# Performance work log

Measured on AMD Instinct MI355X. Metric: run time of the kernel, lower is better.

The kernel has to match this reference:

```python
import jax, jax.numpy as jnp
import numpy as np
from jax import lax

B, N, C, RED = 8, 2048, 1024, 4
GN_EPS = 1e-5


def setup_inputs() -> dict:
    key = jax.random.key(0)
    ks = jax.random.split(key, 8)
    s = lambda k, shp, sc: jax.random.normal(k, shp, jnp.float32) * sc
    return dict(
        x=jax.random.normal(ks[0], (B, N, C), jnp.float32),
        qkv_w=s(ks[1], (C, 3 * C), 0.02),
        c1=jnp.float32(0.01 ** 2),
        c2=jnp.float32(0.03 ** 2),
        conv1_w=s(ks[2], (4, 1, 3), 0.3),      # OIH
        gn_g=jnp.ones(4, jnp.float32),
        gn_b=jnp.zeros(4, jnp.float32),
        conv2_w=s(ks[3], (1, 4, 3), 0.3),      # OIH
        conv2_b=jnp.zeros(1, jnp.float32),
        ch_w1=s(ks[4], (C, C // RED), 0.02),
        ch_b1=jnp.zeros(C // RED, jnp.float32),
        ch_w2=s(ks[5], (C // RED, C), 0.02),
        ch_b2=jnp.zeros(C, jnp.float32),
        proj_w=s(ks[6], (C, C), 0.02),
        proj_b=jnp.zeros(C, jnp.float32),
    )


def _conv1d(x, w):  # x:[B,Cin,N], w:[O,I,3], pad=1
    return lax.conv_general_dilated(x, w, (1,), [(1, 1)],
                                    dimension_numbers=('NCH', 'OIH', 'NCH'))


def _ode_func(A, conv1_w, gn_g, gn_b, conv2_w, conv2_b):
    # A: [B,N] -> Conv1d(1,4) -> GroupNorm(2,4) -> ReLU -> Conv1d(4,1)
    h = _conv1d(A[:, None, :], conv1_w)                 # [B,4,N]
    b, _, n = h.shape
    hg = h.reshape(b, 2, 2, n)                          # 2 groups of 2 channels
    mu = hg.mean((2, 3), keepdims=True)
    var = hg.var((2, 3), keepdims=True)
    h = ((hg - mu) * lax.rsqrt(var + GN_EPS)).reshape(b, 4, n)
    h = jax.nn.relu(h * gn_g[None, :, None] + gn_b[None, :, None])
    y = _conv1d(h, conv2_w) + conv2_b[None, :, None]    # [B,1,N]
    return y[:, 0, :]


def reference(x, qkv_w, c1, c2, conv1_w, gn_g, gn_b, conv2_w, conv2_b,
              ch_w1, ch_b1, ch_w2, ch_b2, proj_w, proj_b):
    Bx, Nx, Cx = x.shape
    qkv = (x @ qkv_w).reshape(Bx, Nx, 3, Cx)
    q, k, v = qkv[..., 0, :], qkv[..., 1, :], qkv[..., 2, :]

    # SSIM-style per-token statistics over the channel dim
    mu_q = q.mean(-1, keepdims=True)
    mu_k = k.mean(-1, keepdims=True)
    dq, dk = q - mu_q, k - mu_k
    inv_cm1 = 1.0 / (Cx - 1)
    sigma_qk = (dq * dk).sum(-1, keepdims=True) * inv_cm1
    sigma_q2 = (dq * dq).sum(-1, keepdims=True) * inv_cm1
    sigma_k2 = (dk * dk).sum(-1, keepdims=True) * inv_cm1
    num = (2 * mu_q * mu_k + c1) * (2 * sigma_qk + c2)
    den = (mu_q ** 2 + mu_k ** 2 + c1) * (sigma_q2 + sigma_k2 + c2)
    attn_base = ((num / (den + 1e-7)) ** 2)[..., 0]     # [B,N]

    # explicit-Euler integration over t = linspace(0,1,2) -> one step, dt=1
    steps = 2
    ts = jnp.linspace(0.0, 1.0, steps)
    dts = ts[1:] - ts[:-1]

    def step(A, dt):
        return A + dt * _ode_func(A, conv1_w, gn_g, gn_b, conv2_w, conv2_b), None

    A, _ = lax.scan(step, attn_base, dts)
    final_a = jax.nn.sigmoid(A)                         # [B,N]
    weights = jax.nn.softmax(final_a, axis=1)           # softmax over tokens

    # channel gating from mean token
    m = x.mean(axis=1, keepdims=True)                   # [B,1,C]
    ch_w = jax.nn.sigmoid(jax.nn.relu(m @ ch_w1 + ch_b1) @ ch_w2 + ch_b2)

    out_low = weights[..., None] * v * ch_w             # [B,N,C]
    return out_low @ proj_w + proj_b
```

## Files before the change

kernel.cpp:

```cpp
#include <hip/hip_runtime.h>

typedef __attribute__((ext_vector_type(8))) short short8;
typedef __attribute__((ext_vector_type(4))) short short4v;
typedef __attribute__((ext_vector_type(4))) float floatx4;

__device__ __forceinline__ unsigned short f2bf(float f) {
    unsigned u = __float_as_uint(f);
    u = u + 0x7fffu + ((u >> 16) & 1u);
    return (unsigned short)(u >> 16);
}
__device__ __forceinline__ float bf2f(short s) {
    return __uint_as_float(((unsigned)(unsigned short)s) << 16);
}

__device__ __forceinline__ void gl_lds16(const void* g, void* l) {
    __builtin_amdgcn_global_load_lds((const __attribute__((address_space(1))) void*)g,
                                     (__attribute__((address_space(3))) void*)l, 16, 0, 0);
}

__global__ __launch_bounds__(256) void convmean_kernel(const float* __restrict__ x,
                                                       short* __restrict__ xb,
                                                       float* __restrict__ part) {
    int bid = blockIdx.x;
    int b = bid >> 6, nch = bid & 63;
    int tid = threadIdx.x;
    size_t base = ((size_t)b * 2048 + nch * 32) * 1024;
    float s0 = 0.f, s1 = 0.f, s2 = 0.f, s3 = 0.f;
    int c0 = tid * 4;
    for (int r = 0; r < 32; r++) {
        const float* rp = x + base + (size_t)r * 1024 + c0;
        float4 v = *(const float4*)rp;
        s0 += v.x; s1 += v.y; s2 += v.z; s3 += v.w;
        short4v o;
        o[0] = (short)f2bf(v.x); o[1] = (short)f2bf(v.y);
        o[2] = (short)f2bf(v.z); o[3] = (short)f2bf(v.w);
        *(short4v*)(xb + base + (size_t)r * 1024 + c0) = o;
    }
    float* pp = part + ((size_t)b * 64 + nch) * 1024 + c0;
    float4 ps; ps.x = s0; ps.y = s1; ps.z = s2; ps.w = s3;
    *(float4*)pp = ps;
}

__global__ __launch_bounds__(256) void transpose_conv_kernel(const float* __restrict__ w_qkv,
                                                             short* __restrict__ qkvT,
                                                             const float* __restrict__ w_proj,
                                                             short* __restrict__ projT) {
    __shared__ float t[64][65];
    int bx = blockIdx.x;
    const float* in; short* out; int C; bool is_qkv;
    int c0, r0 = blockIdx.y * 64;
    if (bx < 48) { in = w_qkv; out = qkvT; C = 3072; c0 = bx * 64; is_qkv = true; }
    else         { in = w_proj; out = projT; C = 1024; c0 = (bx - 48) * 64; is_qkv = false; }
    int tid = threadIdx.x;
#pragma unroll
    for (int l = 0; l < 16; l++) {
        int idx = l * 256 + tid;
        int rr = idx >> 6, cc = idx & 63;
        t[rr][cc] = in[(size_t)(r0 + rr) * C + c0 + cc];
    }
    __syncthreads();
#pragma unroll
    for (int l = 0; l < 16; l++) {
        int idx = l * 256 + tid;
        int rr = idx >> 6, cc = idx & 63;
        int ro = c0 + rr;
        int rnew = ro;
        if (is_qkv) {
            if (ro < 1024) rnew = 2 * ro;
            else if (ro < 2048) rnew = 2 * (ro - 1024) + 1;
        }
        out[(size_t)rnew * 1024 + r0 + cc] = (short)f2bf(t[cc][rr]);
    }
}

__global__ __launch_bounds__(256) void ch_kernel(const float* __restrict__ part,
                                                 const float* __restrict__ w1,
                                                 const float* __restrict__ b1,
                                                 const float* __restrict__ w2,
                                                 const float* __restrict__ b2,
                                                 float* __restrict__ ch) {
    int b = blockIdx.x >> 3, cg = blockIdx.x & 7;
    int tid = threadIdx.x;
    __shared__ float mrow[1024];
    __shared__ float hid[256];
    for (int i = tid; i < 1024; i += 256) {
        float s = 0.f;
        for (int j = 0; j < 64; j++) s += part[((size_t)b * 64 + j) * 1024 + i];
        mrow[i] = s * (1.f / 2048.f);
    }
    __syncthreads();
    {
        float s0 = 0.f, s1 = 0.f, s2 = 0.f, s3 = 0.f;
        for (int i = 0; i < 1024; i += 4) {
            s0 += mrow[i] * w1[(size_t)i * 256 + tid];
            s1 += mrow[i + 1] * w1[(size_t)(i + 1) * 256 + tid];
            s2 += mrow[i + 2] * w1[(size_t)(i + 2) * 256 + tid];
            s3 += mrow[i + 3] * w1[(size_t)(i + 3) * 256 + tid];
        }
        hid[tid] = fmaxf((s0 + s1) + (s2 + s3) + b1[tid], 0.f);
    }
    __syncthreads();
    if (tid < 128) {
        int c = cg * 128 + tid;
        float s0 = 0.f, s1 = 0.f, s2 = 0.f, s3 = 0.f;
        for (int j = 0; j < 256; j += 4) {
            s0 += hid[j] * w2[(size_t)j * 1024 + c];
            s1 += hid[j + 1] * w2[(size_t)(j + 1) * 1024 + c];
            s2 += hid[j + 2] * w2[(size_t)(j + 2) * 1024 + c];
            s3 += hid[j + 3] * w2[(size_t)(j + 3) * 1024 + c];
        }
        float s = (s0 + s1) + (s2 + s3) + b2[c];
        ch[(size_t)b * 1024 + c] = 1.f / (1.f + expf(-s));
    }
}

__global__ __launch_bounds__(256, 4) void gemm_qkv_kernel(const short* __restrict__ A,
                                                          const short* __restrict__ BT,
                                                          short* __restrict__ vbuf,
                                                          const float* __restrict__ ch,
                                                          float* __restrict__ part2)
{
    __shared__ __align__(16) short Ash[2 * 128 * 32];
    __shared__ __align__(16) short Bsh[2 * 128 * 32];
    const int tid = threadIdx.x;
    const int wave = tid >> 6, lane = tid & 63;
    const int id = blockIdx.x;
    const int xcd = id & 7, j = id >> 3;
    const int half = j / 192;
    const int rem = j % 192;
    const int bmi = rem & 7;
    const int bn = rem >> 3;
    const int bm = (half * 8 + bmi) * 8 + xcd;
    const int wm = wave >> 1, wn = wave & 1;
    const int l4 = lane >> 2, kk = (lane & 3) * 8;
    const int lda = 1024, ldb = 1024;

    const short* Ag = A + (size_t)(bm * 128 + wave * 32 + l4) * lda + kk;
    const short* Bg = BT + (size_t)(bn * 128 + wave * 32 + l4) * ldb + kk;
    short* lA = Ash + wave * 1024;
    short* lB = Bsh + wave * 1024;

    floatx4 acc[4][4];
    floatx4 zero = {0.f, 0.f, 0.f, 0.f};
#pragma unroll
    for (int i = 0; i < 4; i++)
#pragma unroll
        for (int jj = 0; jj < 4; jj++) acc[i][jj] = zero;

    const int ar = lane & 15, ak = (lane >> 4) * 8;
    const int quad = lane >> 4;

    for (int k0 = 0; k0 < 1024; k0 += 64) {
#pragma unroll
        for (int h = 0; h < 2; h++) {
            gl_lds16(Ag + k0 + h * 32, lA + h * 4096);
            gl_lds16(Ag + 16 * lda + k0 + h * 32, lA + h * 4096 + 512);
            gl_lds16(Bg + k0 + h * 32, lB + h * 4096);
            gl_lds16(Bg + 16 * ldb + k0 + h * 32, lB + h * 4096 + 512);
        }
        __syncthreads();
#pragma unroll
        for (int h = 0; h < 2; h++) {
            short8 af[4], bfr[4];
#pragma unroll
            for (int t = 0; t < 4; t++)
                af[t] = *(const short8*)(Ash + h * 4096 + (wm * 64 + t * 16 + ar) * 32 + ak);
#pragma unroll
            for (int t = 0; t < 4; t++)
                bfr[t] = *(const short8*)(Bsh + h * 4096 + (wn * 64 + t * 16 + ar) * 32 + ak);
#pragma unroll
            for (int i = 0; i < 4; i++)
#pragma unroll
                for (int jj = 0; jj < 4; jj++)
                    acc[i][jj] = __builtin_amdgcn_mfma_f32_16x16x32_bf16(af[i], bfr[jj], acc[i][jj], 0, 0, 0);
        }
        __syncthreads();
    }

    if (bn < 16) {
        float* sb = (float*)Ash;
#pragma unroll
        for (int i = 0; i < 4; i++) {
            float st[4][5];
#pragma unroll
            for (int r = 0; r < 4; r++)
#pragma unroll
                for (int f = 0; f < 5; f++) st[r][f] = 0.f;
#pragma unroll
            for (int jj = 0; jj < 4; jj++) {
#pragma unroll
                for (int r = 0; r < 4; r++) {
                    float val = acc[i][jj][r];
                    float other = __shfl_xor(val, 1);
                    float q = (lane & 1) ? other : val;
                    float kv = (lane & 1) ? val : other;
                    st[r][0] += q; st[r][1] += kv;
                    st[r][2] += q * q; st[r][3] += kv * kv; st[r][4] += q * kv;
                }
            }
#pragma unroll
            for (int r = 0; r < 4; r++)
#pragma unroll
                for (int f = 0; f < 5; f++) {
                    float v = st[r][f];
                    v += __shfl_xor(v, 2);
                    v += __shfl_xor(v, 4);
                    v += __shfl_xor(v, 8);
                    st[r][f] = v;
                }
            if ((lane & 15) == 0) {
#pragma unroll
                for (int r = 0; r < 4; r++)
#pragma unroll
                    for (int f = 0; f < 5; f++)
                        sb[(size_t)(wn * 128 + wm * 64 + i * 16 + quad * 4 + r) * 5 + f] = st[r][f];
            }
        }
        __syncthreads();
        if (tid < 128) {
            int grow = bm * 128 + tid;
#pragma unroll
            for (int f = 0; f < 5; f++) {
                float s = sb[(size_t)tid * 5 + f] + sb[(size_t)(128 + tid) * 5 + f];
                part2[(size_t)(bn * 5 + f) * 16384 + grow] = s;
            }
        }
    } else {
        const int batch = (bm * 128) >> 11;
        const int vcol0 = bn * 128 - 2048 + wn * 64;
        short* pbuf = Ash + wave * 1024;
        float cw[4];
#pragma unroll
        for (int jj = 0; jj < 4; jj++) cw[jj] = ch[(size_t)batch * 1024 + vcol0 + jj * 16 + ar];
#pragma unroll
        for (int i = 0; i < 4; i++) {
#pragma unroll
            for (int jj = 0; jj < 4; jj++)
#pragma unroll
                for (int r = 0; r < 4; r++)
                    pbuf[(quad * 4 + r) * 64 + jj * 16 + ar] = (short)f2bf(acc[i][jj][r] * cw[jj]);
#pragma unroll
            for (int p = 0; p < 2; p++) {
                int idx = p * 512 + lane * 8;
                short8 vv = *(const short8*)(pbuf + idx);
                int grow = bm * 128 + wm * 64 + i * 16 + (idx >> 6);
                int gcol = vcol0 + (idx & 63);
                *(short8*)(vbuf + (size_t)grow * 1024 + gcol) = vv;
            }
        }
    }
}

__global__ __launch_bounds__(256) void finalize_kernel(const float* __restrict__ part2,
                                                       const float* __restrict__ c1p,
                                                       const float* __restrict__ c2p,
                                                       float* __restrict__ attn) {
    int row = blockIdx.x * 256 + threadIdx.x;
    float s[5] = {0.f, 0.f, 0.f, 0.f, 0.f};
#pragma unroll
    for (int slot = 0; slot < 16; slot++)
#pragma unroll
        for (int f = 0; f < 5; f++)
            s[f] += part2[(size_t)((slot * 5 + f) << 14) + row];
    const float C = 1024.f, invcm1 = 1.f / 1023.f;
    float c1 = *c1p, c2 = *c2p;
    float muq = s[0] / C, muk = s[1] / C;
    float sigqk = (s[4] - C * muq * muk) * invcm1;
    float sigq2 = (s[2] - C * muq * muq) * invcm1;
    float sigk2 = (s[3] - C * muk * muk) * invcm1;
    float num = (2.f * muq * muk + c1) * (2.f * sigqk + c2);
    float den = (muq * muq + muk * muk + c1) * (sigq2 + sigk2 + c2);
    float r = num / (den + 1e-7f);
    attn[row] = r * r;
}

__device__ __forceinline__ float blk_sum(float v, float* buf) {
#pragma unroll
    for (int m = 1; m < 64; m <<= 1) v += __shfl_xor(v, m);
    int wave = threadIdx.x >> 6;
    if ((threadIdx.x & 63) == 0) buf[wave] = v;
    __syncthreads();
    float r = buf[0] + buf[1] + buf[2] + buf[3];
    __syncthreads();
    return r;
}
__device__ __forceinline__ float blk_max(float v, float* buf) {
#pragma unroll
    for (int m = 1; m < 64; m <<= 1) v = fmaxf(v, __shfl_xor(v, m));
    int wave = threadIdx.x >> 6;
    if ((threadIdx.x & 63) == 0) buf[wave] = v;
    __syncthreads();
    float r = fmaxf(fmaxf(buf[0], buf[1]), fmaxf(buf[2], buf[3]));
    __syncthreads();
    return r;
}

__global__ __launch_bounds__(256) void ode_softmax_kernel(const float* __restrict__ attn,
                                                          const float* __restrict__ w1,
                                                          const float* __restrict__ gng,
                                                          const float* __restrict__ gnb,
                                                          const float* __restrict__ w2,
                                                          const float* __restrict__ b2,
                                                          float* __restrict__ wgt) {
    int b = blockIdx.x, tid = threadIdx.x;
    __shared__ float A0[2048];
    __shared__ float H[4][2048];
    __shared__ float rbuf[4];
    for (int i = tid; i < 2048; i += 256) A0[i] = attn[(size_t)b * 2048 + i];
    __syncthreads();
    float w1l[12], w2l[12];
#pragma unroll
    for (int i = 0; i < 12; i++) { w1l[i] = w1[i]; w2l[i] = w2[i]; }
    float gg[4], gb[4];
#pragma unroll
    for (int c = 0; c < 4; c++) { gg[c] = gng[c]; gb[c] = gnb[c]; }

    float s0 = 0.f, ss0 = 0.f, s1 = 0.f, ss1 = 0.f;
    for (int i = tid; i < 2048; i += 256) {
        float le = (i > 0) ? A0[i - 1] : 0.f;
        float mi = A0[i];
        float ri = (i < 2047) ? A0[i + 1] : 0.f;
#pragma unroll
        for (int c = 0; c < 4; c++) {
            float h = w1l[c * 3] * le + w1l[c * 3 + 1] * mi + w1l[c * 3 + 2] * ri;
            H[c][i] = h;
            if (c < 2) { s0 += h; ss0 += h * h; } else { s1 += h; ss1 += h * h; }
        }
    }
    s0 = blk_sum(s0, rbuf);
    ss0 = blk_sum(ss0, rbuf);
    s1 = blk_sum(s1, rbuf);
    ss1 = blk_sum(ss1, rbuf);
    float mu0 = s0 / 4096.f, var0 = ss0 / 4096.f - mu0 * mu0;
    float mu1 = s1 / 4096.f, var1 = ss1 / 4096.f - mu1 * mu1;
    float is0 = 1.f / sqrtf(var0 + 1e-5f);
    float is1 = 1.f / sqrtf(var1 + 1e-5f);

    for (int i = tid; i < 2048; i += 256) {
#pragma unroll
        for (int c = 0; c < 4; c++) {
            float inv = (c < 2) ? is0 : is1;
            float mu = (c < 2) ? mu0 : mu1;
            float v = (H[c][i] - mu) * inv * gg[c] + gb[c];
            H[c][i] = fmaxf(v, 0.f);
        }
    }
    __syncthreads();

    float bias2 = b2[0];
    float myfa[8];
    float lmax = -1e30f;
#pragma unroll
    for (int ii = 0; ii < 8; ii++) {
        int i = tid + ii * 256;
        float y = bias2;
#pragma unroll
        for (int c = 0; c < 4; c++) {
            float le = (i > 0) ? H[c][i - 1] : 0.f;
            float mi = H[c][i];
            float ri = (i < 2047) ? H[c][i + 1] : 0.f;
            y += w2l[c * 3] * le + w2l[c * 3 + 1] * mi + w2l[c * 3 + 2] * ri;
        }
        float Av = A0[i] + y;
        float fa = 1.f / (1.f + expf(-Av));
        myfa[ii] = fa;
        lmax = fmaxf(lmax, fa);
    }
    float gmax = blk_max(lmax, rbuf);
    float lsum = 0.f;
#pragma unroll
    for (int ii = 0; ii < 8; ii++) {
        myfa[ii] = expf(myfa[ii] - gmax);
        lsum += myfa[ii];
    }
    float gsum = blk_sum(lsum, rbuf);
    float inv = 1.f / gsum;
#pragma unroll
    for (int ii = 0; ii < 8; ii++) wgt[(size_t)b * 2048 + tid + ii * 256] = myfa[ii] * inv;
}

__global__ __launch_bounds__(256, 4) void gemm_out_kernel(const short* __restrict__ vbuf,
                                                          const short* __restrict__ BT,
                                                          const float* __restrict__ wgt,
                                                          const float* __restrict__ pb,
                                                          float* __restrict__ Out)
{
    __shared__ __align__(16) short Ash[2 * 128 * 32];
    __shared__ __align__(16) short Bsh[2 * 128 * 32];
    const int tid = threadIdx.x;
    const int wave = tid >> 6, lane = tid & 63;
    const int id = blockIdx.x;
    const int xcd = id & 7, j = id >> 3;
    const int half = j >> 6;
    const int rem = j & 63;
    const int bmi = rem & 7;
    const int bn = rem >> 3;
    const int bm = (half * 8 + bmi) * 8 + xcd;
    const int wm = wave >> 1, wn = wave & 1;
    const int l4 = lane >> 2, kk = (lane & 3) * 8;
    const int lda = 1024, ldb = 1024;

    const short* Ag = vbuf + (size_t)(bm * 128 + wave * 32 + l4) * lda + kk;
    const short* Bg = BT + (size_t)(bn * 128 + wave * 32 + l4) * ldb + kk;
    short* lA = Ash + wave * 1024;
    short* lB = Bsh + wave * 1024;

    floatx4 acc[4][4];
    floatx4 zero = {0.f, 0.f, 0.f, 0.f};
#pragma unroll
    for (int i = 0; i < 4; i++)
#pragma unroll
        for (int jj = 0; jj < 4; jj++) acc[i][jj] = zero;

    const int ar = lane & 15, ak = (lane >> 4) * 8;
    const int quad = lane >> 4;

    for (int k0 = 0; k0 < 1024; k0 += 64) {
#pragma unroll
        for (int h = 0; h < 2; h++) {
            gl_lds16(Ag + k0 + h * 32, lA + h * 4096);
            gl_lds16(Ag + 16 * lda + k0 + h * 32, lA + h * 4096 + 512);
            gl_lds16(Bg + k0 + h * 32, lB + h * 4096);
            gl_lds16(Bg + 16 * ldb + k0 + h * 32, lB + h * 4096 + 512);
        }
        __syncthreads();
#pragma unroll
        for (int h = 0; h < 2; h++) {
            short8 af[4], bfr[4];
#pragma unroll
            for (int t = 0; t < 4; t++)
                af[t] = *(const short8*)(Ash + h * 4096 + (wm * 64 + t * 16 + ar) * 32 + ak);
#pragma unroll
            for (int t = 0; t < 4; t++)
                bfr[t] = *(const short8*)(Bsh + h * 4096 + (wn * 64 + t * 16 + ar) * 32 + ak);
#pragma unroll
            for (int i = 0; i < 4; i++)
#pragma unroll
                for (int jj = 0; jj < 4; jj++)
                    acc[i][jj] = __builtin_amdgcn_mfma_f32_16x16x32_bf16(af[i], bfr[jj], acc[i][jj], 0, 0, 0);
        }
        __syncthreads();
    }

    const int row0 = bm * 128 + wm * 64;
    const int col0 = bn * 128 + wn * 64;
    float* obuf = (float*)Ash + wave * 1024;
#pragma unroll
    for (int i = 0; i < 4; i++) {
#pragma unroll
        for (int jj = 0; jj < 4; jj++) {
            float bias = pb[col0 + jj * 16 + ar];
#pragma unroll
            for (int r = 0; r < 4; r++) {
                int grow = row0 + i * 16 + quad * 4 + r;
                obuf[(quad * 4 + r) * 64 + jj * 16 + ar] = wgt[grow] * acc[i][jj][r] + bias;
            }
        }
#pragma unroll
        for (int p = 0; p < 4; p++) {
            int idx = p * 256 + lane * 4;
            float4 vv = *(const float4*)(obuf + idx);
            int grow = row0 + i * 16 + (idx >> 6);
            int gcol = col0 + (idx & 63);
            *(float4*)(Out + (size_t)grow * 1024 + gcol) = vv;
        }
    }
}

extern "C" void kernel_launch(void* const* d_in, const int* in_sizes, int n_in,
                              void* d_out, int out_size, void* d_ws, size_t ws_size,
                              hipStream_t stream) {
    const float* x       = (const float*)d_in[0];
    const float* qkv_w   = (const float*)d_in[1];
    const float* c1      = (const float*)d_in[2];
    const float* c2      = (const float*)d_in[3];
    const float* conv1_w = (const float*)d_in[4];
    const float* gn_g    = (const float*)d_in[5];
    const float* gn_b    = (const float*)d_in[6];
    const float* conv2_w = (const float*)d_in[7];
    const float* conv2_b = (const float*)d_in[8];
    const float* ch_w1   = (const float*)d_in[9];
    const float* ch_b1   = (const float*)d_in[10];
    const float* ch_w2   = (const float*)d_in[11];
    const float* ch_b2   = (const float*)d_in[12];
    const float* proj_w  = (const float*)d_in[13];
    const float* proj_b  = (const float*)d_in[14];
    float* out = (float*)d_out;

    size_t off = 0;
    char* base = (char*)d_ws;
    auto carve = [&](size_t bytes) -> char* {
        char* p = base + off;
        off += (bytes + 255) & ~(size_t)255;
        return p;
    };
    short* x_bf  = (short*)carve((size_t)16384 * 1024 * 2);
    short* qkvT  = (short*)carve((size_t)3072 * 1024 * 2);
    short* projT = (short*)carve((size_t)1024 * 1024 * 2);
    short* vbuf  = (short*)carve((size_t)16384 * 1024 * 2);
    float* part2 = (float*)carve((size_t)80 * 16384 * 4);
    float* attn  = (float*)carve((size_t)16384 * 4);
    float* wgt   = (float*)carve((size_t)16384 * 4);
    float* part  = (float*)carve((size_t)8 * 64 * 1024 * 4);
    float* chw   = (float*)carve((size_t)8 * 1024 * 4);

    convmean_kernel<<<512, 256, 0, stream>>>(x, x_bf, part);
    transpose_conv_kernel<<<dim3(64, 16), 256, 0, stream>>>(qkv_w, qkvT, proj_w, projT);
    ch_kernel<<<64, 256, 0, stream>>>(part, ch_w1, ch_b1, ch_w2, ch_b2, chw);
    gemm_qkv_kernel<<<3072, 256, 0, stream>>>(x_bf, qkvT, vbuf, chw, part2);
    finalize_kernel<<<64, 256, 0, stream>>>(part2, c1, c2, attn);
    ode_softmax_kernel<<<8, 256, 0, stream>>>(attn, conv1_w, gn_g, gn_b, conv2_w, conv2_b, wgt);
    gemm_out_kernel<<<1024, 256, 0, stream>>>(vbuf, projT, wgt, proj_b, out);
}
```

Measured before the change: 387.3 us.

## Fold V projection and channel gate into per-batch output weight matrix

Rather than computing V = x@Wv for all tokens and then projecting, the code precomputes a per-batch matrix M_b = Wv·diag(ch_b)·Wproj (8 small 1024^3 GEMMs) and multiplies x directly by it in the output GEMM. The QKV GEMM shrinks to Q and K only, and the bf16 V buffer write and read are gone. The cost is extra small GEMMs plus an added bf16 rounding of the fused matrix, which changes numerical error characteristics.

```diff
diff --git a/kernel.cpp b/kernel.cpp
--- a/kernel.cpp
+++ b/kernel.cpp
@@ -8,9 +8,6 @@
     unsigned u = __float_as_uint(f);
     u = u + 0x7fffu + ((u >> 16) & 1u);
     return (unsigned short)(u >> 16);
-}
-__device__ __forceinline__ float bf2f(short s) {
-    return __uint_as_float(((unsigned)(unsigned short)s) << 16);
 }
 
 __device__ __forceinline__ void gl_lds16(const void* g, void* l) {
@@ -49,8 +46,8 @@
     int bx = blockIdx.x;
     const float* in; short* out; int C; bool is_qkv;
     int c0, r0 = blockIdx.y * 64;
-    if (bx < 48) { in = w_qkv; out = qkvT; C = 3072; c0 = bx * 64; is_qkv = true; }
-    else         { in = w_proj; out = projT; C = 1024; c0 = (bx - 48) * 64; is_qkv = false; }
+    if (bx < 32) { in = w_qkv; out = qkvT; C = 3072; c0 = bx * 64; is_qkv = true; }
+    else         { in = w_proj; out = projT; C = 1024; c0 = (bx - 32) * 64; is_qkv = false; }
     int tid = threadIdx.x;
 #pragma unroll
     for (int l = 0; l < 16; l++) {
@@ -65,10 +62,7 @@
         int rr = idx >> 6, cc = idx & 63;
         int ro = c0 + rr;
         int rnew = ro;
-        if (is_qkv) {
-            if (ro < 1024) rnew = 2 * ro;
-            else if (ro < 2048) rnew = 2 * (ro - 1024) + 1;
-        }
+        if (is_qkv) rnew = (ro < 1024) ? 2 * ro : 2 * (ro - 1024) + 1;
         out[(size_t)rnew * 1024 + r0 + cc] = (short)f2bf(t[cc][rr]);
     }
 }
@@ -114,11 +108,106 @@
     }
 }
 
-__global__ __launch_bounds__(256, 4) void gemm_qkv_kernel(const short* __restrict__ A,
-                                                          const short* __restrict__ BT,
-                                                          short* __restrict__ vbuf,
-                                                          const float* __restrict__ ch,
-                                                          float* __restrict__ part2)
+__global__ __launch_bounds__(256) void scale_wv_kernel(const float* __restrict__ qkv_w,
+                                                       const float* __restrict__ ch,
+                                                       short* __restrict__ WvB) {
+    int m = blockIdx.x, tid = threadIdx.x;
+    int c0 = tid * 4;
+    float4 wv = *(const float4*)(qkv_w + (size_t)m * 3072 + 2048 + c0);
+#pragma unroll
+    for (int b = 0; b < 8; b++) {
+        float4 cv = *(const float4*)(ch + (size_t)b * 1024 + c0);
+        short4v o;
+        o[0] = (short)f2bf(wv.x * cv.x);
+        o[1] = (short)f2bf(wv.y * cv.y);
+        o[2] = (short)f2bf(wv.z * cv.z);
+        o[3] = (short)f2bf(wv.w * cv.w);
+        *(short4v*)(WvB + (((size_t)b << 20) + (size_t)m * 1024 + c0)) = o;
+    }
+}
+
+__global__ __launch_bounds__(256, 4) void mb_gemm_kernel(const short* __restrict__ projT,
+                                                         const short* __restrict__ WvB,
+                                                         short* __restrict__ MbT)
+{
+    __shared__ __align__(16) short Ash[2 * 128 * 32];
+    __shared__ __align__(16) short Bsh[2 * 128 * 32];
+    const int tid = threadIdx.x;
+    const int wave = tid >> 6, lane = tid & 63;
+    const int id = blockIdx.x;
+    const int b = id >> 6, t = id & 63;
+    const int bmj = t >> 3, bnc = t & 7;
+    const int wm = wave >> 1, wn = wave & 1;
+    const int l4 = lane >> 2, kk = (lane & 3) * 8;
+
+    const short* Bbase = WvB + ((size_t)b << 20);
+    const short* Ag = projT + (size_t)(bmj * 128 + wave * 32 + l4) * 1024 + kk;
+    const short* Bg = Bbase + (size_t)(bnc * 128 + wave * 32 + l4) * 1024 + kk;
+    short* lA = Ash + wave * 1024;
+    short* lB = Bsh + wave * 1024;
+
+    floatx4 acc[4][4];
+    floatx4 zero = {0.f, 0.f, 0.f, 0.f};
+#pragma unroll
+    for (int i = 0; i < 4; i++)
+#pragma unroll
+        for (int jj = 0; jj < 4; jj++) acc[i][jj] = zero;
+
+    const int ar = lane & 15, ak = (lane >> 4) * 8;
+    const int quad = lane >> 4;
+
+    for (int k0 = 0; k0 < 1024; k0 += 64) {
+#pragma unroll
+        for (int h = 0; h < 2; h++) {
+            gl_lds16(Ag + k0 + h * 32, lA + h * 4096);
+            gl_lds16(Ag + 16 * 1024 + k0 + h * 32, lA + h * 4096 + 512);
+            gl_lds16(Bg + k0 + h * 32, lB + h * 4096);
+            gl_lds16(Bg + 16 * 1024 + k0 + h * 32, lB + h * 4096 + 512);
+        }
+        __syncthreads();
+#pragma unroll
+        for (int h = 0; h < 2; h++) {
+            short8 af[4], bfr[4];
+#pragma unroll
+            for (int t2 = 0; t2 < 4; t2++)
+                af[t2] = *(const short8*)(Ash + h * 4096 + (wm * 64 + t2 * 16 + ar) * 32 + ak);
+#pragma unroll
+            for (int t2 = 0; t2 < 4; t2++)
+                bfr[t2] = *(const short8*)(Bsh + h * 4096 + (wn * 64 + t2 * 16 + ar) * 32 + ak);
+#pragma unroll
+            for (int i = 0; i < 4; i++)
+#pragma unroll
+                for (int jj = 0; jj < 4; jj++)
+                    acc[i][jj] = __builtin_amdgcn_mfma_f32_16x16x32_bf16(af[i], bfr[jj], acc[i][jj], 0, 0, 0);
+        }
+        __syncthreads();
+    }
+
+    short* pbuf = Ash + wave * 1024;
+    const int row0 = bmj * 128 + wm * 64;
+    const int col0 = bnc * 128 + wn * 64;
+    short* obase = MbT + ((size_t)b << 20);
+#pragma unroll
+    for (int i = 0; i < 4; i++) {
+#pragma unroll
+        for (int jj = 0; jj < 4; jj++)
+#pragma unroll
+            for (int r = 0; r < 4; r++)
+                pbuf[(quad * 4 + r) * 64 + jj * 16 + ar] = (short)f2bf(acc[i][jj][r]);
+#pragma unroll
+        for (int p = 0; p < 2; p++) {
+            int idx = p * 512 + lane * 8;
+            short8 vv = *(const short8*)(pbuf + idx);
+            int grow = row0 + i * 16 + (idx >> 6);
+            int gcol = col0 + (idx & 63);
+            *(short8*)(obase + (size_t)grow * 1024 + gcol) = vv;
+        }
+    }
+}
+
+__global__ __launch_bounds__(256, 4) void gemm_qk_kernel(const short* __restrict__ A,
+                                                         const short* __restrict__ BT,
+                                                         float* __restrict__ part2)
 {
     __shared__ __align__(16) short Ash[2 * 128 * 32];
     __shared__ __align__(16) short Bsh[2 * 128 * 32];
@@ -126,17 +215,16 @@
     const int wave = tid >> 6, lane = tid & 63;
     const int id = blockIdx.x;
     const int xcd = id & 7, j = id >> 3;
-    const int half = j / 192;
-    const int rem = j % 192;
+    const int half = j >> 7;
+    const int rem = j & 127;
     const int bmi = rem & 7;
     const int bn = rem >> 3;
     const int bm = (half * 8 + bmi) * 8 + xcd;
     const int wm = wave >> 1, wn = wave & 1;
     const int l4 = lane >> 2, kk = (lane & 3) * 8;
-    const int lda = 1024, ldb = 1024;
-
-    const short* Ag = A + (size_t)(bm * 128 + wave * 32 + l4) * lda + kk;
-    const short* Bg = BT + (size_t)(bn * 128 + wave * 32 + l4) * ldb + kk;
+
+    const short* Ag = A + (size_t)(bm * 128 + wave * 32 + l4) * 1024 + kk;
+    const short* Bg = BT + (size_t)(bn * 128 + wave * 32 + l4) * 1024 + kk;
     short* lA = Ash + wave * 1024;
     short* lB = Bsh + wave * 1024;
 
@@ -154,9 +242,9 @@
 #pragma unroll
         for (int h = 0; h < 2; h++) {
             gl_lds16(Ag + k0 + h * 32, lA + h * 4096);
-            gl_lds16(Ag + 16 * lda + k0 + h * 32, lA + h * 4096 + 512);
+            gl_lds16(Ag + 16 * 1024 + k0 + h * 32, lA + h * 4096 + 512);
             gl_lds16(Bg + k0 + h * 32, lB + h * 4096);
-            gl_lds16(Bg + 16 * ldb + k0 + h * 32, lB + h * 4096 + 512);
+            gl_lds16(Bg + 16 * 1024 + k0 + h * 32, lB + h * 4096 + 512);
         }
         __syncthreads();
 #pragma unroll
@@ -177,76 +265,51 @@
         __syncthreads();
     }
 
-    if (bn < 16) {
-        float* sb = (float*)Ash;
-#pragma unroll
-        for (int i = 0; i < 4; i++) {
-            float st[4][5];
+    float* sb = (float*)Ash;
+#pragma unroll
+    for (int i = 0; i < 4; i++) {
+        float st[4][5];
+#pragma unroll
+        for (int r = 0; r < 4; r++)
+#pragma unroll
+            for (int f = 0; f < 5; f++) st[r][f] = 0.f;
+#pragma unroll
+        for (int jj = 0; jj < 4; jj++) {
+#pragma unroll
+            for (int r = 0; r < 4; r++) {
+                float val = acc[i][jj][r];
+                float other = __shfl_xor(val, 1);
+                float q = (lane & 1) ? other : val;
+                float kv = (lane & 1) ? val : other;
+                st[r][0] += q; st[r][1] += kv;
+                st[r][2] += q * q; st[r][3] += kv * kv; st[r][4] += q * kv;
+            }
+        }
+#pragma unroll
+        for (int r = 0; r < 4; r++)
+#pragma unroll
+            for (int f = 0; f < 5; f++) {
+                float v = st[r][f];
+                v += __shfl_xor(v, 2);
+                v += __shfl_xor(v, 4);
+                v += __shfl_xor(v, 8);
+                st[r][f] = v;
+            }
+        if ((lane & 15) == 0) {
 #pragma unroll
             for (int r = 0; r < 4; r++)
 #pragma unroll
-                for (int f = 0; f < 5; f++) st[r][f] = 0.f;
-#pragma unroll
-            for (int jj = 0; jj < 4; jj++) {
-#pragma unroll
-                for (int r = 0; r < 4; r++) {
-                    float val = acc[i][jj][r];
-                    float other = __shfl_xor(val, 1);
-                    float q = (lane & 1) ? other : val;
-                    float kv = (lane & 1) ? val : other;
-                    st[r][0] += q; st[r][1] += kv;
-                    st[r][2] += q * q; st[r][3] += kv * kv; st[r][4] += q * kv;
-                }
-            }
-#pragma unroll
-            for (int r = 0; r < 4; r++)
-#pragma unroll
-                for (int f = 0; f < 5; f++) {
-                    float v = st[r][f];
-                    v += __shfl_xor(v, 2);
-                    v += __shfl_xor(v, 4);
-                    v += __shfl_xor(v, 8);
-                    st[r][f] = v;
-                }
-            if ((lane & 15) == 0) {
-#pragma unroll
-                for (int r = 0; r < 4; r++)
-#pragma unroll
-                    for (int f = 0; f < 5; f++)
-                        sb[(size_t)(wn * 128 + wm * 64 + i * 16 + quad * 4 + r) * 5 + f] = st[r][f];
-            }
-        }
-        __syncthreads();
-        if (tid < 128) {
-            int grow = bm * 128 + tid;
-#pragma unroll
-            for (int f = 0; f < 5; f++) {
-                float s = sb[(size_t)tid * 5 + f] + sb[(size_t)(128 + tid) * 5 + f];
-                part2[(size_t)(bn * 5 + f) * 16384 + grow] = s;
-            }
-        }
-    } else {
-        const int batch = (bm * 128) >> 11;
-        const int vcol0 = bn * 128 - 2048 + wn * 64;
-        short* pbuf = Ash + wave * 1024;
-        float cw[4];
-#pragma unroll
-        for (int jj = 0; jj < 4; jj++) cw[jj] = ch[(size_t)batch * 1024 + vcol0 + jj * 16 + ar];
-#pragma unroll
-        for (int i = 0; i < 4; i++) {
-#pragma unroll
-            for (int jj = 0; jj < 4; jj++)
-#pragma unroll
-                for (int r = 0; r < 4; r++)
-                    pbuf[(quad * 4 + r) * 64 + jj * 16 + ar] = (short)f2bf(acc[i][jj][r] * cw[jj]);
-#pragma unroll
-            for (int p = 0; p < 2; p++) {
-                int idx = p * 512 + lane * 8;
-                short8 vv = *(const short8*)(pbuf + idx);
-                int grow = bm * 128 + wm * 64 + i * 16 + (idx >> 6);
-                int gcol = vcol0 + (idx & 63);
-                *(short8*)(vbuf + (size_t)grow * 1024 + gcol) = vv;
-            }
+                for (int f = 0; f < 5; f++)
+                    sb[(size_t)(wn * 128 + wm * 64 + i * 16 + quad * 4 + r) * 5 + f] = st[r][f];
+        }
+    }
+    __syncthreads();
+    if (tid < 128) {
+        int grow = bm * 128 + tid;
+#pragma unroll
+        for (int f = 0; f < 5; f++) {
+            float s = sb[(size_t)tid * 5 + f] + sb[(size_t)(128 + tid) * 5 + f];
+            part2[(size_t)(bn * 5 + f) * 16384 + grow] = s;
         }
     }
 }
@@ -379,8 +442,8 @@
     for (int ii = 0; ii < 8; ii++) wgt[(size_t)b * 2048 + tid + ii * 256] = myfa[ii] * inv;
 }
 
-__global__ __launch_bounds__(256, 4) void gemm_out_kernel(const short* __restrict__ vbuf,
-                                                          const short* __restrict__ BT,
+__global__ __launch_bounds__(256, 4) void gemm_out_kernel(const short* __restrict__ A,
+                                                          const short* __restrict__ MbT,
                                                           const float* __restrict__ wgt,
                                                           const float* __restrict__ pb,
                                                           float* __restrict__ Out)
@@ -396,12 +459,13 @@
     const int bmi = rem & 7;
     const int bn = rem >> 3;
     const int bm = (half * 8 + bmi) * 8 + xcd;
+    const int batch = bm >> 4;
     const int wm = wave >> 1, wn = wave & 1;
     const int l4 = lane >> 2, kk = (lane & 3) * 8;
-    const int lda = 1024, ldb = 1024;
-
-    const short* Ag = vbuf + (size_t)(bm * 128 + wave * 32 + l4) * lda + kk;
-    const short* Bg = BT + (size_t)(bn * 128 + wave * 32 + l4) * ldb + kk;
+
+    const short* BT = MbT + ((size_t)batch << 20);
+    const short* Ag = A + (size_t)(bm * 128 + wave * 32 + l4) * 1024 + kk;
+    const short* Bg = BT + (size_t)(bn * 128 + wave * 32 + l4) * 1024 + kk;
     short* lA = Ash + wave * 1024;
     short* lB = Bsh + wave * 1024;
 
@@ -419,9 +483,9 @@
 #pragma unroll
         for (int h = 0; h < 2; h++) {
             gl_lds16(Ag + k0 + h * 32, lA + h * 4096);
-            gl_lds16(Ag + 16 * lda + k0 + h * 32, lA + h * 4096 + 512);
+            gl_lds16(Ag + 16 * 1024 + k0 + h * 32, lA + h * 4096 + 512);
             gl_lds16(Bg + k0 + h * 32, lB + h * 4096);
-            gl_lds16(Bg + 16 * ldb + k0 + h * 32, lB + h * 4096 + 512);
+            gl_lds16(Bg + 16 * 1024 + k0 + h * 32, lB + h * 4096 + 512);
         }
         __syncthreads();
 #pragma unroll
@@ -495,9 +559,10 @@
         return p;
     };
     short* x_bf  = (short*)carve((size_t)16384 * 1024 * 2);
-    short* qkvT  = (short*)carve((size_t)3072 * 1024 * 2);
+    short* qkvT  = (short*)carve((size_t)2048 * 1024 * 2);
     short* projT = (short*)carve((size_t)1024 * 1024 * 2);
-    short* vbuf  = (short*)carve((size_t)16384 * 1024 * 2);
+    short* WvB   = (short*)carve((size_t)8 * 1024 * 1024 * 2);
+    short* MbT   = (short*)carve((size_t)8 * 1024 * 1024 * 2);
     float* part2 = (float*)carve((size_t)80 * 16384 * 4);
     float* attn  = (float*)carve((size_t)16384 * 4);
     float* wgt   = (float*)carve((size_t)16384 * 4);
@@ -505,10 +570,12 @@
     float* chw   = (float*)carve((size_t)8 * 1024 * 4);
 
     convmean_kernel<<<512, 256, 0, stream>>>(x, x_bf, part);
-    transpose_conv_kernel<<<dim3(64, 16), 256, 0, stream>>>(qkv_w, qkvT, proj_w, projT);
+    transpose_conv_kernel<<<dim3(48, 16), 256, 0, stream>>>(qkv_w, qkvT, proj_w, projT);
     ch_kernel<<<64, 256, 0, stream>>>(part, ch_w1, ch_b1, ch_w2, ch_b2, chw);
-    gemm_qkv_kernel<<<3072, 256, 0, stream>>>(x_bf, qkvT, vbuf, chw, part2);
+    scale_wv_kernel<<<1024, 256, 0, stream>>>(qkv_w, chw, WvB);
+    mb_gemm_kernel<<<512, 256, 0, stream>>>(projT, WvB, MbT);
+    gemm_qk_kernel<<<2048, 256, 0, stream>>>(x_bf, qkvT, part2);
     finalize_kernel<<<64, 256, 0, stream>>>(part2, c1, c2, attn);
     ode_softmax_kernel<<<8, 256, 0, stream>>>(attn, conv1_w, gn_g, gn_b, conv2_w, conv2_b, wgt);
-    gemm_out_kernel<<<1024, 256, 0, stream>>>(vbuf, projT, wgt, proj_b, out);
-}
+    gemm_out_kernel<<<1024, 256, 0, stream>>>(x_bf, MbT, wgt, proj_b, out);
+}
```

Result: slower. 406.3 us (+4.9%).
